# Optimization experiments

Hardware: AMD Instinct MI355X
Metric: run time of the kernel (lower is better)

The kernel has to match this reference:

```python
import jax, jax.numpy as jnp
import numpy as np

N_NODES = 50000
N_EDGES = 800000
N_GRAPHS = 16
F_IN = 128
E_DIM = 16
HID = 32
HEADS = 2
EPS_BN = 1e-5


def gatv2_conv(x, edge_index, edge_attr, Wl, bl, Wr, br, We, att, bias, heads, out_ch):
    """PyG GATv2Conv (share_weights=False, concat=True, add_self_loops=True, fill_value='mean')."""
    n = x.shape[0]
    src, dst = edge_index[0], edge_index[1]
    loop = jnp.arange(n)
    src = jnp.concatenate([src, loop])
    dst = jnp.concatenate([dst, loop])
    ea = jnp.concatenate([edge_attr, jnp.broadcast_to(edge_attr.mean(0), (n, edge_attr.shape[1]))])
    x_l = (x @ Wl + bl).reshape(n, heads, out_ch)   # source transform
    x_r = (x @ Wr + br).reshape(n, heads, out_ch)   # target transform
    e = (ea @ We).reshape(-1, heads, out_ch)
    m = jax.nn.leaky_relu(x_l[src] + x_r[dst] + e, 0.2)      # [E, H, C]
    alpha = (m * att[None]).sum(-1)                          # [E, H]
    amax = jax.ops.segment_max(alpha, dst, num_segments=n)
    ex = jnp.exp(alpha - amax[dst])
    denom = jax.ops.segment_sum(ex, dst, num_segments=n)
    alpha = ex / (denom[dst] + 1e-16)
    out = jax.ops.segment_sum(x_l[src] * alpha[..., None], dst, num_segments=n)
    return out.reshape(n, heads * out_ch) + bias


def batch_norm(x, g, b):
    mu = x.mean(0)
    var = jnp.var(x, axis=0)  # biased, as torch BatchNorm1d training mode
    return (x - mu) * jax.lax.rsqrt(var + EPS_BN) * g + b


def setup_inputs() -> dict:
    key = jax.random.key(0)
    ks = jax.random.split(key, 24)
    s = 0.1
    d1 = HID * HEADS  # 64
    inp = {
        'x': jax.random.normal(ks[0], (N_NODES, F_IN), jnp.float32),
        'edge_index': jax.random.randint(ks[1], (2, N_EDGES), 0, N_NODES),
        'edge_attr': jax.random.normal(ks[2], (N_EDGES, E_DIM), jnp.float32),
        'batch': jnp.sort(jax.random.randint(ks[3], (N_NODES,), 0, N_GRAPHS)),
        'skip1_W': jax.random.normal(ks[4], (F_IN, d1)) * s,
        'skip1_b': jnp.zeros((d1,)),
        'conv1_Wl': jax.random.normal(ks[5], (F_IN, d1)) * s,
        'conv1_bl': jnp.zeros((d1,)),
        'conv1_Wr': jax.random.normal(ks[6], (F_IN, d1)) * s,
        'conv1_br': jnp.zeros((d1,)),
        'conv1_We': jax.random.normal(ks[7], (E_DIM, d1)) * s,
        'conv1_att': jax.random.normal(ks[8], (HEADS, HID)) * s,
        'conv1_bias': jnp.zeros((d1,)),
        'bn1_g': jnp.ones((d1,)),
        'bn1_b': jnp.zeros((d1,)),
        'skip2_W': jax.random.normal(ks[9], (d1, HID)) * s,
        'skip2_b': jnp.zeros((HID,)),
        'conv2_Wl': jax.random.normal(ks[10], (d1, HID)) * s,
        'conv2_bl': jnp.zeros((HID,)),
        'conv2_Wr': jax.random.normal(ks[11], (d1, HID)) * s,
        'conv2_br': jnp.zeros((HID,)),
        'conv2_We': jax.random.normal(ks[12], (E_DIM, HID)) * s,
        'conv2_att': jax.random.normal(ks[13], (1, HID)) * s,
        'conv2_bias': jnp.zeros((HID,)),
        'bn2_g': jnp.ones((HID,)),
        'bn2_b': jnp.zeros((HID,)),
    }
    return inp


def reference(x, edge_index, edge_attr, batch,
              skip1_W, skip1_b, conv1_Wl, conv1_bl, conv1_Wr, conv1_br, conv1_We, conv1_att, conv1_bias, bn1_g, bn1_b,
              skip2_W, skip2_b, conv2_Wl, conv2_bl, conv2_Wr, conv2_br, conv2_We, conv2_att, conv2_bias, bn2_g, bn2_b):
    h_proj = x @ skip1_W + skip1_b
    h = gatv2_conv(x, edge_index, edge_attr, conv1_Wl, conv1_bl, conv1_Wr, conv1_br, conv1_We, conv1_att, conv1_bias, HEADS, HID)
    h = jax.nn.elu(batch_norm(h, bn1_g, bn1_b) + h_proj)
    h_proj = h @ skip2_W + skip2_b
    h2 = gatv2_conv(h, edge_index, edge_attr, conv2_Wl, conv2_bl, conv2_Wr, conv2_br, conv2_We, conv2_att, conv2_bias, 1, HID)
    h2 = jax.nn.elu(batch_norm(h2, bn2_g, bn2_b) + h_proj)
    ones = jnp.ones((h2.shape[0],), h2.dtype)
    counts = jax.ops.segment_sum(ones, batch, num_segments=N_GRAPHS)
    x_mean = jax.ops.segment_sum(h2, batch, num_segments=N_GRAPHS) / jnp.maximum(counts, 1.0)[:, None]
    x_max = jax.ops.segment_max(h2, batch, num_segments=N_GRAPHS)
    x_max = jnp.where(counts[:, None] > 0, x_max, 0.0)
    return jnp.concatenate([x_mean, x_max], axis=1)
```

## Files before the change

kernel.cpp:

```cpp
#include <hip/hip_runtime.h>
#include <hip/hip_bf16.h>

#define NE 800000
#define NN 50000
#define NG 16
#define ETOT (NE + NN)

typedef unsigned short u16;
typedef __attribute__((ext_vector_type(8))) short short8;
typedef __attribute__((ext_vector_type(4))) float float4v;

__device__ __forceinline__ float b2f(u16 u) {
  return __uint_as_float(((unsigned)u) << 16);
}
__device__ __forceinline__ u16 f2b(float f) {
  __hip_bfloat16 b = __float2bfloat16(f);
  return *(u16*)&b;
}
__device__ __forceinline__ void cv8(uint4 v, float* o) {
  o[0] = __uint_as_float(v.x << 16);
  o[1] = __uint_as_float(v.x & 0xFFFF0000u);
  o[2] = __uint_as_float(v.y << 16);
  o[3] = __uint_as_float(v.y & 0xFFFF0000u);
  o[4] = __uint_as_float(v.z << 16);
  o[5] = __uint_as_float(v.z & 0xFFFF0000u);
  o[6] = __uint_as_float(v.w << 16);
  o[7] = __uint_as_float(v.w & 0xFFFF0000u);
}
__device__ __forceinline__ unsigned pk2(float a, float b) {
  return (unsigned)f2b(a) | ((unsigned)f2b(b) << 16);
}
__device__ __forceinline__ unsigned f2key(float f) {
  unsigned u = __float_as_uint(f);
  return (u & 0x80000000u) ? ~u : (u | 0x80000000u);
}
__device__ __forceinline__ float key2f(unsigned k) {
  unsigned u = (k & 0x80000000u) ? (k ^ 0x80000000u) : ~k;
  return __uint_as_float(u);
}
__device__ __forceinline__ int plaus(unsigned h) {
  unsigned eh = (h >> 7) & 0xFF;
  return (h == 0) || (eh >= 100 && eh <= 140);
}
__device__ __forceinline__ float lrelu(float v) {
  return (v > 0.f) ? v : 0.2f * v;
}

__global__ __launch_bounds__(256) void k_init(uint4* __restrict__ zbase, int zcnt16,
                                              const unsigned* __restrict__ a,
                                              const unsigned* __restrict__ b,
                                              const unsigned* __restrict__ c,
                                              int* __restrict__ flags) {
  uint4 z = {0, 0, 0, 0};
  for (int i = blockIdx.x * 256 + threadIdx.x; i < zcnt16; i += gridDim.x * 256)
    zbase[i] = z;
  if (blockIdx.x != 0) return;
  __shared__ int cnt[3];
  if (threadIdx.x < 3) cnt[threadIdx.x] = 0;
  __syncthreads();
  const unsigned* arr[3] = {a, b, c};
  for (int k = 0; k < 3; k++) {
    int ok = 0;
    for (int i = threadIdx.x; i < 4096; i += 256) {
      unsigned w = arr[k][i];
      ok += (plaus(w & 0xFFFFu) && plaus(w >> 16)) ? 1 : 0;
    }
    atomicAdd(&cnt[k], ok);
  }
  __syncthreads();
  if (threadIdx.x == 0) {
    int f0 = cnt[0] > 2048, f1 = cnt[1] > 2048, f2 = cnt[2] > 2048;
    flags[0] = f0;
    flags[1] = f1;
    flags[2] = f2;
    flags[3] = f0 && f1 && f2;
  }
}

__global__ __launch_bounds__(256) void k_histcol(const int* __restrict__ ei,
                                                 const void* __restrict__ ea,
                                                 const int* __restrict__ flg,
                                                 int* __restrict__ deg4,
                                                 float* __restrict__ mean_part) {
  int gt = blockIdx.x * 256 + threadIdx.x;
  if (gt < ETOT) {
    int dst = (gt < NE) ? ei[NE + gt] : gt - NE;
    atomicAdd(&deg4[(blockIdx.x & 3) * NN + dst], 1);
  }
  bool eb = flg[2] != 0;
  int col = gt & 15;
  int row = gt >> 4;
  int rstride = (gridDim.x * 256) >> 4;
  float s = 0.f;
  if (eb) {
    const u16* p = (const u16*)ea;
    for (int e = row; e < NE; e += rstride) s += b2f(p[(size_t)e * 16 + col]);
  } else {
    const float* p = (const float*)ea;
    for (int e = row; e < NE; e += rstride) s += p[(size_t)e * 16 + col];
  }
  __shared__ float ls[256];
  ls[threadIdx.x] = s;
  __syncthreads();
  if (threadIdx.x < 16) {
    float t = 0.f;
    for (int i = threadIdx.x; i < 256; i += 16) t += ls[i];
    atomicAdd(&mean_part[(blockIdx.x & 63) * 16 + threadIdx.x], t);
  }
}

template <int K, int N>
__device__ __forceinline__ void load_W_f32(float* Wf, const void* W, bool wb) {
  if (wb) {
    const u16* Wp = (const u16*)W;
    for (int i = threadIdx.x; i < K * N / 8; i += 256) {
      float t[8];
      cv8(*(const uint4*)(Wp + i * 8), t);
#pragma unroll
      for (int q = 0; q < 8; q++) Wf[i * 8 + q] = t[q];
    }
  } else {
    const float* Wp = (const float*)W;
    for (int i = threadIdx.x; i < K * N / 4; i += 256) {
      float4 v = *(const float4*)(Wp + i * 4);
      Wf[i * 4 + 0] = v.x; Wf[i * 4 + 1] = v.y;
      Wf[i * 4 + 2] = v.z; Wf[i * 4 + 3] = v.w;
    }
  }
}

template <int K, int N, int RPB>
__device__ __forceinline__ void gemm_mfma_tile(
    const float* __restrict__ Wf,
    const void* __restrict__ xin, bool xb, bool wb,
    const void* __restrict__ bb, u16* __restrict__ out, int tile) {
  constexpr int CT = N / 16;
  constexpr int WPC = 4 / CT;
  constexpr int KK = K / 32;
  int lane = threadIdx.x & 63;
  int wave = threadIdx.x >> 6;
  int col = lane & 15;
  int quad = lane >> 4;
  int ct = wave % CT;
  int rt_off = wave / CT;
  short8 bh[KK], bl[KK];
#pragma unroll
  for (int kk = 0; kk < KK; kk++) {
    short8 th, tl;
#pragma unroll
    for (int j = 0; j < 8; j++) {
      float w = Wf[(kk * 32 + quad * 8 + j) * N + ct * 16 + col];
      u16 hb = f2b(w);
      th[j] = (short)hb;
      tl[j] = (short)f2b(w - b2f(hb));
    }
    bh[kk] = th;
    bl[kk] = tl;
  }
  float bias = wb ? b2f(((const u16*)bb)[ct * 16 + col])
                  : ((const float*)bb)[ct * 16 + col];
  int rt0 = tile * RPB;
  for (int i = rt_off; i < RPB; i += WPC) {
    int rt = rt0 + i;
    int row = rt * 16 + col;
    float4v acc = {0.f, 0.f, 0.f, 0.f};
    if (xb) {
      const u16* xp = (const u16*)xin;
#pragma unroll
      for (int kk = 0; kk < KK; kk++) {
        short8 af = *(const short8*)(xp + (size_t)row * K + kk * 32 + quad * 8);
        acc = __builtin_amdgcn_mfma_f32_16x16x32_bf16(af, bh[kk], acc, 0, 0, 0);
        if (!wb)
          acc = __builtin_amdgcn_mfma_f32_16x16x32_bf16(af, bl[kk], acc, 0, 0, 0);
      }
    } else {
      const float* xp = (const float*)xin;
#pragma unroll
      for (int kk = 0; kk < KK; kk++) {
        float4 v0 = *(const float4*)(xp + (size_t)row * K + kk * 32 + quad * 8);
        float4 v1 = *(const float4*)(xp + (size_t)row * K + kk * 32 + quad * 8 + 4);
        float a[8] = {v0.x, v0.y, v0.z, v0.w, v1.x, v1.y, v1.z, v1.w};
        short8 ah, al;
#pragma unroll
        for (int j = 0; j < 8; j++) {
          u16 hb = f2b(a[j]);
          ah[j] = (short)hb;
          al[j] = (short)f2b(a[j] - b2f(hb));
        }
        acc = __builtin_amdgcn_mfma_f32_16x16x32_bf16(ah, bh[kk], acc, 0, 0, 0);
        acc = __builtin_amdgcn_mfma_f32_16x16x32_bf16(al, bh[kk], acc, 0, 0, 0);
        if (!wb)
          acc = __builtin_amdgcn_mfma_f32_16x16x32_bf16(ah, bl[kk], acc, 0, 0, 0);
      }
    }
#pragma unroll
    for (int r = 0; r < 4; r++) {
      int orow = rt * 16 + quad * 4 + r;
      out[(size_t)orow * N + ct * 16 + col] = f2b(acc[r] + bias);
    }
  }
}

template <int K, int N, int TILES, int RPB>
__global__ __launch_bounds__(256) void k_scanlin1(
    const int* __restrict__ deg4, int* __restrict__ start, int* __restrict__ cursor,
    const float* __restrict__ mean_part, float* __restrict__ mean_sums,
    const void* __restrict__ xin, const int* __restrict__ flg,
    const void* W0, const void* W1, const void* W2,
    const void* b0, const void* b1, const void* b2,
    u16* __restrict__ o0, u16* __restrict__ o1, u16* __restrict__ o2, int M) {
  (void)M;
  __shared__ __align__(16) float smem[K * N];

  if ((int)blockIdx.x == 0) {
    int t = threadIdx.x;
    if (t < 16) {
      float s = 0.f;
#pragma unroll
      for (int j = 0; j < 64; j++) s += mean_part[j * 16 + t];
      mean_sums[t] = s;
    }
    constexpr int NT = (NN + 1023) / 1024;
    int* ws = (int*)smem;
    int* tbase = ws + 256;
    int lane = t & 63;
    int wv = t >> 6;
    for (int tile = 0; tile < NT; tile++) {
      int idx = tile * 1024 + t * 4;
      int4 d = {0, 0, 0, 0};
      if (idx + 3 < NN) {
#pragma unroll
        for (int c = 0; c < 4; c++) {
          int4 dc = *(const int4*)(deg4 + c * NN + idx);
          d.x += dc.x; d.y += dc.y; d.z += dc.z; d.w += dc.w;
        }
      } else {
#pragma unroll
        for (int c = 0; c < 4; c++) {
          if (idx + 0 < NN) d.x += deg4[c * NN + idx + 0];
          if (idx + 1 < NN) d.y += deg4[c * NN + idx + 1];
          if (idx + 2 < NN) d.z += deg4[c * NN + idx + 2];
          if (idx + 3 < NN) d.w += deg4[c * NN + idx + 3];
        }
      }
      int s4 = d.x + d.y + d.z + d.w;
      int r = s4;
#pragma unroll
      for (int ofs = 1; ofs < 64; ofs <<= 1) r += __shfl_xor(r, ofs, 64);
      if (lane == 0) ws[tile * 4 + wv] = r;
    }
    __syncthreads();
    if (wv == 0) {
      int g0 = 0, g1 = 0, g2 = 0, g3 = 0;
      if (lane < NT) {
        g0 = ws[lane * 4 + 0];
        g1 = ws[lane * 4 + 1];
        g2 = ws[lane * 4 + 2];
        g3 = ws[lane * 4 + 3];
      }
      int gs = g0 + g1 + g2 + g3;
      int sc = gs;
#pragma unroll
      for (int ofs = 1; ofs < 64; ofs <<= 1) {
        int v = __shfl_up(sc, ofs, 64);
        if (lane >= ofs) sc += v;
      }
      int base = sc - gs;
      if (lane < NT) {
        tbase[lane * 4 + 0] = base;
        tbase[lane * 4 + 1] = base + g0;
        tbase[lane * 4 + 2] = base + g0 + g1;
        tbase[lane * 4 + 3] = base + g0 + g1 + g2;
      }
      if (lane == NT - 1) start[NN] = base + gs;
    }
    __syncthreads();
    for (int tile = 0; tile < NT; tile++) {
      int idx = tile * 1024 + t * 4;
      int4 d = {0, 0, 0, 0};
      if (idx + 3 < NN) {
#pragma unroll
        for (int c = 0; c < 4; c++) {
          int4 dc = *(const int4*)(deg4 + c * NN + idx);
          d.x += dc.x; d.y += dc.y; d.z += dc.z; d.w += dc.w;
        }
      } else {
#pragma unroll
        for (int c = 0; c < 4; c++) {
          if (idx + 0 < NN) d.x += deg4[c * NN + idx + 0];
          if (idx + 1 < NN) d.y += deg4[c * NN + idx + 1];
          if (idx + 2 < NN) d.z += deg4[c * NN + idx + 2];
          if (idx + 3 < NN) d.w += deg4[c * NN + idx + 3];
        }
      }
      int s4 = d.x + d.y + d.z + d.w;
      int sc = s4;
#pragma unroll
      for (int ofs = 1; ofs < 64; ofs <<= 1) {
        int v = __shfl_up(sc, ofs, 64);
        if (lane >= ofs) sc += v;
      }
      int excl = tbase[tile * 4 + wv] + (sc - s4);
      int4 st;
      st.x = excl;
      st.y = excl + d.x;
      st.z = st.y + d.y;
      st.w = st.z + d.z;
      if (idx + 3 < NN) {
        *(int4*)(start + idx) = st;
        *(int4*)(cursor + idx) = st;
      } else {
        if (idx + 0 < NN) { start[idx + 0] = st.x; cursor[idx + 0] = st.x; }
        if (idx + 1 < NN) { start[idx + 1] = st.y; cursor[idx + 1] = st.y; }
        if (idx + 2 < NN) { start[idx + 2] = st.z; cursor[idx + 2] = st.z; }
        if (idx + 3 < NN) { start[idx + 3] = st.w; cursor[idx + 3] = st.w; }
      }
    }
    return;
  }
  int lidx = blockIdx.x - 1;
  int wset = lidx / TILES;
  int tile = lidx % TILES;
  bool wb = flg[1] != 0;
  bool xb = flg[0] != 0;
  const void* W = wset == 0 ? W0 : (wset == 1 ? W1 : W2);
  const void* bb = wset == 0 ? b0 : (wset == 1 ? b1 : b2);
  u16* out = wset == 0 ? o0 : (wset == 1 ? o1 : o2);
  load_W_f32<K, N>(smem, W, wb);
  __syncthreads();
  gemm_mfma_tile<K, N, RPB>(smem, xin, xb, wb, bb, out, tile);
}

__global__ __launch_bounds__(256) void k_buildcsr_pay(
    const int* __restrict__ ei, const void* __restrict__ eattr,
    const int* __restrict__ flg, const float* __restrict__ mean_sums,
    int* __restrict__ cursor, int* __restrict__ csr_src,
    u16* __restrict__ ea16) {
  int e = blockIdx.x * 256 + threadIdx.x;
  if (e >= ETOT) return;
  bool eb = flg[2] != 0;
  int src, dst;
  if (e < NE) { src = ei[e]; dst = ei[NE + e]; } else { src = dst = e - NE; }
  float rec[16];
  if (e < NE) {
    if (eb) {
      const uint4* q = (const uint4*)((const u16*)eattr + (size_t)e * 16);
      cv8(q[0], rec);
      cv8(q[1], rec + 8);
    } else {
      const float* q = (const float*)eattr + (size_t)e * 16;
#pragma unroll
      for (int k = 0; k < 16; k++) rec[k] = q[k];
    }
  } else {
#pragma unroll
    for (int k = 0; k < 16; k++) rec[k] = mean_sums[k] * (1.0f / NE);
  }
  int pos = atomicAdd(&cursor[dst], 1);
  csr_src[pos] = src;
  u16 rb[16];
#pragma unroll
  for (int k = 0; k < 16; k++) rb[k] = f2b(rec[k]);
  uint4* dp = (uint4*)(ea16 + (size_t)pos * 16);
  dp[0] = *(uint4*)rb;
  dp[1] = *(uint4*)(rb + 8);
}

__global__ __launch_bounds__(256) void k_buildcsr(const int* __restrict__ ei,
                                                  int* __restrict__ cursor,
                                                  uint2* __restrict__ csr) {
  int e = blockIdx.x * 256 + threadIdx.x;
  if (e >= ETOT) return;
  int src, dst;
  if (e < NE) { src = ei[e]; dst = ei[NE + e]; } else { src = dst = e - NE; }
  int pos = atomicAdd(&cursor[dst], 1);
  uint2 r; r.x = (unsigned)src; r.y = (unsigned)e;
  csr[pos] = r;
}

__global__ __launch_bounds__(256) void k_ewgemm(
    const u16* __restrict__ ea, const int* __restrict__ flg,
    const void* We1, const void* We2,
    u16* __restrict__ ew1, u16* __restrict__ ew2) {
  bool wb = flg[1] != 0;
  int lane = threadIdx.x & 63;
  int col = lane & 15;
  int quad = lane >> 4;
  short8 b1h[4], b1l[4], b2h[2], b2l[2];
#pragma unroll
  for (int ct = 0; ct < 4; ct++) {
    short8 th, tl;
#pragma unroll
    for (int j = 0; j < 8; j++) {
      int k = quad * 8 + j;
      float w = 0.f;
      if (k < 16)
        w = wb ? b2f(((const u16*)We1)[k * 64 + ct * 16 + col])
               : ((const float*)We1)[k * 64 + ct * 16 + col];
      u16 hb = f2b(w);
      th[j] = (short)hb;
      tl[j] = (short)f2b(w - b2f(hb));
    }
    b1h[ct] = th; b1l[ct] = tl;
  }
#pragma unroll
  for (int ct = 0; ct < 2; ct++) {
    short8 th, tl;
#pragma unroll
    for (int j = 0; j < 8; j++) {
      int k = quad * 8 + j;
      float w = 0.f;
      if (k < 16)
        w = wb ? b2f(((const u16*)We2)[k * 32 + ct * 16 + col])
               : ((const float*)We2)[k * 32 + ct * 16 + col];
      u16 hb = f2b(w);
      th[j] = (short)hb;
      tl[j] = (short)f2b(w - b2f(hb));
    }
    b2h[ct] = th; b2l[ct] = tl;
  }
  int nw = (gridDim.x * 256) >> 6;
  int wid = (blockIdx.x * 256 + threadIdx.x) >> 6;
  const int NT = ETOT / 16;
  for (int rt = wid; rt < NT; rt += nw) {
    int row = rt * 16 + col;
    short8 af = {0, 0, 0, 0, 0, 0, 0, 0};
    if (quad < 2) af = *(const short8*)(ea + (size_t)row * 16 + quad * 8);
#pragma unroll
    for (int ct = 0; ct < 4; ct++) {
      float4v acc = {0.f, 0.f, 0.f, 0.f};
      acc = __builtin_amdgcn_mfma_f32_16x16x32_bf16(af, b1h[ct], acc, 0, 0, 0);
      acc = __builtin_amdgcn_mfma_f32_16x16x32_bf16(af, b1l[ct], acc, 0, 0, 0);
#pragma unroll
      for (int r = 0; r < 4; r++)
        ew1[(size_t)(rt * 16 + quad * 4 + r) * 64 + ct * 16 + col] = f2b(acc[r]);
    }
#pragma unroll
    for (int ct = 0; ct < 2; ct++) {
      float4v acc = {0.f, 0.f, 0.f, 0.f};
      acc = __builtin_amdgcn_mfma_f32_16x16x32_bf16(af, b2h[ct], acc, 0, 0, 0);
      acc = __builtin_amdgcn_mfma_f32_16x16x32_bf16(af, b2l[ct], acc, 0, 0, 0);
#pragma unroll
      for (int r = 0; r < 4; r++)
        ew2[(size_t)(rt * 16 + quad * 4 + r) * 32 + ct * 16 + col] = f2b(acc[r]);
    }
  }
}

template <int K, int N, int RPB>
__global__ __launch_bounds__(256) void k_lin3b(
    const void* __restrict__ xin, const int* __restrict__ flg,
    const void* W0, const void* W1, const void* W2,
    const void* b0, const void* b1, const void* b2,
    u16* __restrict__ o0, u16* __restrict__ o1, u16* __restrict__ o2, int M) {
  (void)M;
  __shared__ __align__(16) float smem[K * N];
  bool wb = flg[1] != 0;
  const void* W = blockIdx.y == 0 ? W0 : (blockIdx.y == 1 ? W1 : W2);
  const void* bb = blockIdx.y == 0 ? b0 : (blockIdx.y == 1 ? b1 : b2);
  u16* out = blockIdx.y == 0 ? o0 : (blockIdx.y == 1 ? o1 : o2);
  load_W_f32<K, N>(smem, W, wb);
  __syncthreads();
  gemm_mfma_tile<K, N, RPB>(smem, xin, true, wb, bb, out, blockIdx.x);
}

__device__ __forceinline__ float dot16b(const u16* __restrict__ p,
                                        const float* __restrict__ W) {
  float ea[16];
  const uint4* q = (const uint4*)p;
  cv8(q[0], ea);
  cv8(q[1], ea + 8);
  float s = 0.f;
#pragma unroll
  for (int k = 0; k < 16; k++) s += ea[k] * W[k];
  return s;
}
__device__ __forceinline__ float dot16u(const u16* __restrict__ p,
                                        const float* __restrict__ W) {
  const uint4* q = (const uint4*)p;
  uint4 A = q[0], B = q[1];
  unsigned w0 = (unsigned)__builtin_amdgcn_readfirstlane((int)A.x);
  unsigned w1 = (unsigned)__builtin_amdgcn_readfirstlane((int)A.y);
  unsigned w2 = (unsigned)__builtin_amdgcn_readfirstlane((int)A.z);
  unsigned w3 = (unsigned)__builtin_amdgcn_readfirstlane((int)A.w);
  unsigned w4 = (unsigned)__builtin_amdgcn_readfirstlane((int)B.x);
  unsigned w5 = (unsigned)__builtin_amdgcn_readfirstlane((int)B.y);
  unsigned w6 = (unsigned)__builtin_amdgcn_readfirstlane((int)B.z);
  unsigned w7 = (unsigned)__builtin_amdgcn_readfirstlane((int)B.w);
  float s = 0.f;
  s += __uint_as_float(w0 << 16) * W[0];
  s += __uint_as_float(w0 & 0xFFFF0000u) * W[1];
  s += __uint_as_float(w1 << 16) * W[2];
  s += __uint_as_float(w1 & 0xFFFF0000u) * W[3];
  s += __uint_as_float(w2 << 16) * W[4];
  s += __uint_as_float(w2 & 0xFFFF0000u) * W[5];
  s += __uint_as_float(w3 << 16) * W[6];
  s += __uint_as_float(w3 & 0xFFFF0000u) * W[7];
  s += __uint_as_float(w4 << 16) * W[8];
  s += __uint_as_float(w4 & 0xFFFF0000u) * W[9];
  s += __uint_as_float(w5 << 16) * W[10];
  s += __uint_as_float(w5 & 0xFFFF0000u) * W[11];
  s += __uint_as_float(w6 << 16) * W[12];
  s += __uint_as_float(w6 & 0xFFFF0000u) * W[13];
  s += __uint_as_float(w7 << 16) * W[14];
  s += __uint_as_float(w7 & 0xFFFF0000u) * W[15];
  return s;
}
__device__ __forceinline__ float dot16f(const float* __restrict__ q,
                                        const float* __restrict__ W) {
  float s = 0.f;
#pragma unroll
  for (int k = 0; k < 16; k++) s += q[k] * W[k];
  return s;
}

template <int H, int C, bool PRE>
__global__ __launch_bounds__(256) void k_fusedp(
    const int* __restrict__ start, const int* __restrict__ csr_src,
    const u16* __restrict__ pay, const u16* __restrict__ ewp,
    const int* __restrict__ flg,
    const u16* __restrict__ xl, const u16* __restrict__ xr,
    const void* We, const void* att, u16* __restrict__ agg) {
  constexpr int D = H * C;
  constexpr int NPW = 64 / D;
  bool wb = flg[1] != 0;
  int lane = threadIdx.x & 63;
  int ch = lane % D;
  float Wreg[16];
  if constexpr (!PRE) {
    if (wb) {
      const u16* Wp = (const u16*)We;
#pragma unroll
      for (int k = 0; k < 16; k++) Wreg[k] = b2f(Wp[k * D + ch]);
    } else {
      const float* Wp = (const float*)We;
#pragma unroll
      for (int k = 0; k < 16; k++) Wreg[k] = Wp[k * D + ch];
    }
  }
  float attv = wb ? b2f(((const u16*)att)[ch]) : ((const float*)att)[ch];
  int wid = (blockIdx.x * 256 + threadIdx.x) >> 6;

  if constexpr (NPW == 1) {
    int node = __builtin_amdgcn_readfirstlane(wid);
    int s0 = __builtin_amdgcn_readfirstlane(start[node]);
    int s1 = __builtin_amdgcn_readfirstlane(start[node + 1]);
    float xrv = b2f(xr[(unsigned)node * D + ch]);
    float ssum = 0.f, acc = 0.f;
    int p = s0;
    for (; p + 3 < s1; p += 4) {
      int c0 = __builtin_amdgcn_readfirstlane(csr_src[p + 0]);
      int c1 = __builtin_amdgcn_readfirstlane(csr_src[p + 1]);
      int c2 = __builtin_amdgcn_readfirstlane(csr_src[p + 2]);
      int c3 = __builtin_amdgcn_readfirstlane(csr_src[p + 3]);
      float xlv0 = b2f(xl[(unsigned)c0 * D + ch]);
      float xlv1 = b2f(xl[(unsigned)c1 * D + ch]);
      float xlv2 = b2f(xl[(unsigned)c2 * D + ch]);
      float xlv3 = b2f(xl[(unsigned)c3 * D + ch]);
      float ev0, ev1, ev2, ev3;
      if constexpr (PRE) {
        ev0 = b2f(ewp[(size_t)(p + 0) * D + ch]);
        ev1 = b2f(ewp[(size_t)(p + 1) * D + ch]);
        ev2 = b2f(ewp[(size_t)(p + 2) * D + ch]);
        ev3 = b2f(ewp[(size_t)(p + 3) * D + ch]);
      } else {
        ev0 = dot16u(pay + (size_t)(p + 0) * 16, Wreg);
        ev1 = dot16u(pay + (size_t)(p + 1) * 16, Wreg);
        ev2 = dot16u(pay + (size_t)(p + 2) * 16, Wreg);
        ev3 = dot16u(pay + (size_t)(p + 3) * 16, Wreg);
      }
      float t0 = lrelu(xlv0 + xrv + ev0) * attv;
      float t1 = lrelu(xlv1 + xrv + ev1) * attv;
      float t2 = lrelu(xlv2 + xrv + ev2) * attv;
      float t3 = lrelu(xlv3 + xrv + ev3) * attv;
#pragma unroll
      for (int mk = 1; mk <= 16; mk <<= 1) {
        t0 += __shfl_xor(t0, mk, 64);
        t1 += __shfl_xor(t1, mk, 64);
        t2 += __shfl_xor(t2, mk, 64);
        t3 += __shfl_xor(t3, mk, 64);
      }
      float ex0 = __expf(t0);
      float ex1 = __expf(t1);
      float ex2 = __expf(t2);
      float ex3 = __expf(t3);
      ssum += (ex0 + ex1) + (ex2 + ex3);
      acc += ex0 * xlv0 + ex1 * xlv1;
      acc += ex2 * xlv2 + ex3 * xlv3;
    }
    for (; p < s1; ++p) {
      int c0 = __builtin_amdgcn_readfirstlane(csr_src[p]);
      float xlv = b2f(xl[(unsigned)c0 * D + ch]);
      float ev;
      if constexpr (PRE) ev = b2f(ewp[(size_t)p * D + ch]);
      else ev = dot16u(pay + (size_t)p * 16, Wreg);
      float t = lrelu(xlv + xrv + ev) * attv;
#pragma unroll
      for (int mk = 1; mk <= 16; mk <<= 1) t += __shfl_xor(t, mk, 64);
      float ex = __expf(t);
      ssum += ex;
      acc += ex * xlv;
    }
    agg[(size_t)node * D + ch] = f2b(acc / (ssum + 1e-16f));
  } else {
    int node = wid * NPW + lane / D;
    int s0 = start[node], s1 = start[node + 1];
    int deg = s1 - s0;
    int last = s1 - 1;
    int degmax = max(deg, __shfl_xor(deg, 32, 64));
    float xrv = b2f(xr[(unsigned)node * D + ch]);
    float ssum = 0.f, acc = 0.f;
    for (int i = 0; i < degmax; i += 4) {
      int p0 = min(s0 + i + 0, last);
      int p1 = min(s0 + i + 1, last);
      int p2 = min(s0 + i + 2, last);
      int p3 = min(s0 + i + 3, last);
      bool a0 = i + 0 < deg, a1 = i + 1 < deg, a2 = i + 2 < deg, a3 = i + 3 < deg;
      int c0 = csr_src[p0];
      int c1 = csr_src[p1];
      int c2 = csr_src[p2];
      int c3 = csr_src[p3];
      float xlv0 = b2f(xl[(unsigned)c0 * D + ch]);
      float xlv1 = b2f(xl[(unsigned)c1 * D + ch]);
      float xlv2 = b2f(xl[(unsigned)c2 * D + ch]);
      float xlv3 = b2f(xl[(unsigned)c3 * D + ch]);
      float ev0, ev1, ev2, ev3;
      if constexpr (PRE) {
        ev0 = b2f(ewp[(size_t)p0 * D + ch]);
        ev1 = b2f(ewp[(size_t)p1 * D + ch]);
        ev2 = b2f(ewp[(size_t)p2 * D + ch]);
        ev3 = b2f(ewp[(size_t)p3 * D + ch]);
      } else {
        ev0 = dot16b(pay + (size_t)p0 * 16, Wreg);
        ev1 = dot16b(pay + (size_t)p1 * 16, Wreg);
        ev2 = dot16b(pay + (size_t)p2 * 16, Wreg);
        ev3 = dot16b(pay + (size_t)p3 * 16, Wreg);
      }
      float t0 = lrelu(xlv0 + xrv + ev0) * attv;
      float t1 = lrelu(xlv1 + xrv + ev1) * attv;
      float t2 = lrelu(xlv2 + xrv + ev2) * attv;
      float t3 = lrelu(xlv3 + xrv + ev3) * attv;
#pragma unroll
      for (int mk = 1; mk <= 16; mk <<= 1) {
        t0 += __shfl_xor(t0, mk, 64);
        t1 += __shfl_xor(t1, mk, 64);
        t2 += __shfl_xor(t2, mk, 64);
        t3 += __shfl_xor(t3, mk, 64);
      }
      float ex0 = a0 ? __expf(t0) : 0.f;
      float ex1 = a1 ? __expf(t1) : 0.f;
      float ex2 = a2 ? __expf(t2) : 0.f;
      float ex3 = a3 ? __expf(t3) : 0.f;
      ssum += (ex0 + ex1) + (ex2 + ex3);
      acc += ex0 * xlv0 + ex1 * xlv1;
      acc += ex2 * xlv2 + ex3 * xlv3;
    }
    agg[(size_t)node * D + ch] = f2b(acc / (ssum + 1e-16f));
  }
}

template <int H, int C>
__global__ __launch_bounds__(256) void k_fusedg(
    const int* __restrict__ start, const uint2* __restrict__ csr,
    const void* __restrict__ eattr, const int* __restrict__ flg,
    const float* __restrict__ mean_sums,
    const u16* __restrict__ xl, const u16* __restrict__ xr,
    const void* We, const void* att, u16* __restrict__ agg) {
  constexpr int D = H * C;
  constexpr int NPW = 64 / D;
  bool wb = flg[1] != 0;
  bool eb = flg[2] != 0;
  int lane = threadIdx.x & 63;
  int ch = lane % D;
  float Wreg[16];
  if (wb) {
    const u16* Wp = (const u16*)We;
#pragma unroll
    for (int k = 0; k < 16; k++) Wreg[k] = b2f(Wp[k * D + ch]);
  } else {
    const float* Wp = (const float*)We;
#pragma unroll
    for (int k = 0; k < 16; k++) Wreg[k] = Wp[k * D + ch];
  }
  float attv = wb ? b2f(((const u16*)att)[ch]) : ((const float*)att)[ch];
  float ev_self = 0.f;
#pragma unroll
  for (int k = 0; k < 16; k++) ev_self += mean_sums[k] * (1.0f / NE) * Wreg[k];
  int wid = (blockIdx.x * 256 + threadIdx.x) >> 6;
  int node = wid * NPW + lane / D;
  int s0 = start[node], s1 = start[node + 1];
  int deg = s1 - s0;
  int last = s1 - 1;
  int degmax = deg;
  if constexpr (NPW == 2) degmax = max(deg, __shfl_xor(deg, 32, 64));
  float xrv = b2f(xr[(size_t)node * D + ch]);
  float ssum = 0.f, acc = 0.f;
  for (int i = 0; i < degmax; i += 2) {
    uint2 cr0 = csr[min(s0 + i, last)];
    uint2 cr1 = csr[min(s0 + i + 1, last)];
    bool a0 = i < deg, a1 = i + 1 < deg;
    float xlv0 = b2f(xl[(size_t)cr0.x * D + ch]);
    float xlv1 = b2f(xl[(size_t)cr1.x * D + ch]);
    float ev0 = cr0.y < NE ? (eb ? dot16b((const u16*)eattr + (size_t)cr0.y * 16, Wreg)
                                 : dot16f((const float*)eattr + (size_t)cr0.y * 16, Wreg))
                           : ev_self;
    float ev1 = cr1.y < NE ? (eb ? dot16b((const u16*)eattr + (size_t)cr1.y * 16, Wreg)
                                 : dot16f((const float*)eattr + (size_t)cr1.y * 16, Wreg))
                           : ev_self;
    float mv0 = xlv0 + xrv + ev0;
    float mv1 = xlv1 + xrv + ev1;
    mv0 = (mv0 > 0.f) ? mv0 : 0.2f * mv0;
    mv1 = (mv1 > 0.f) ? mv1 : 0.2f * mv1;
    float t0 = mv0 * attv, t1 = mv1 * attv;
#pragma unroll
    for (int mk = 1; mk <= 16; mk <<= 1) {
      t0 += __shfl_xor(t0, mk, 64);
      t1 += __shfl_xor(t1, mk, 64);
    }
    float ex0 = a0 ? __expf(t0) : 0.f;
    float ex1 = a1 ? __expf(t1) : 0.f;
    ssum += ex0 + ex1;
    acc += ex0 * xlv0 + ex1 * xlv1;
  }
  agg[(size_t)node * D + ch] = f2b(acc / (ssum + 1e-16f));
}

template <int D>
__global__ __launch_bounds__(256) void k_bnred(const u16* __restrict__ v,
                                               float* __restrict__ sum,
                                               float* __restrict__ sq, int M) {
  constexpr int RB = 256 / D;
  int tid = threadIdx.x;
  int c = tid % D;
  int rg = tid / D;
  float s = 0.f, q = 0.f;
  for (int r = blockIdx.x * RB + rg; r < M; r += gridDim.x * RB) {
    float x = b2f(v[(size_t)r * D + c]);
    s += x;
    q += x * x;
  }
  __shared__ float ls[256], lq[256];
  ls[tid] = s; lq[tid] = q;
  __syncthreads();
  if (tid < D) {
    float ts = 0.f, tq = 0.f;
    for (int i = tid; i < 256; i += D) { ts += ls[i]; tq += lq[i]; }
    atomicAdd(&sum[tid], ts);
    atomicAdd(&sq[tid], tq);
  }
}

template <int D>
__global__ __launch_bounds__(256) void k_bnapply(const u16* __restrict__ agg,
                                                 const u16* __restrict__ hp,
                                                 const float* __restrict__ sum,
                                                 const float* __restrict__ sq,
                                                 const void* g, const void* b,
                                                 const int* __restrict__ flg,
                                                 u16* __restrict__ out, int M) {
  bool wb = flg[1] != 0;
  int idx = blockIdx.x * 256 + threadIdx.x;
  if (idx >= M * D) return;
  int c = idx & (D - 1);
  float gc = wb ? b2f(((const u16*)g)[c]) : ((const float*)g)[c];
  float bc = wb ? b2f(((const u16*)b)[c]) : ((const float*)b)[c];
  float mu = sum[c] * (1.f / M);
  float var = fmaxf(sq[c] * (1.f / M) - mu * mu, 0.f);
  float sc = rsqrtf(var + 1e-5f) * gc;
  float v = (b2f(agg[idx]) - mu) * sc + bc + b2f(hp[idx]);
  v = v > 0.f ? v : expm1f(v);
  out[idx] = f2b(v);
}

__global__ __launch_bounds__(256) void k_poolall(
    const u16* __restrict__ agg2, const u16* __restrict__ hp2,
    const float* __restrict__ sum, const float* __restrict__ sq,
    const void* g, const void* b, const int* __restrict__ flg,
    const int* __restrict__ batch,
    float* __restrict__ pool_sum, unsigned* __restrict__ pool_maxk,
    float* __restrict__ pool_cnt, int* __restrict__ done_cnt,
    void* __restrict__ out) {
  bool wb = flg[1] != 0;
  int c = threadIdx.x & 31;
  int rg = threadIdx.x >> 5;
  float gc = wb ? b2f(((const u16*)g)[c]) : ((const float*)g)[c];
  float bc = wb ? b2f(((const u16*)b)[c]) : ((const float*)b)[c];
  float mu = sum[c] * (1.f / NN);
  float var = fmaxf(sq[c] * (1.f / NN) - mu * mu, 0.f);
  float scl = rsqrtf(var + 1e-5f) * gc;
  float sh = bc - mu * scl;

  const int NPB = 256;
  int n0 = blockIdx.x * NPB;
  int nend = min(n0 + NPB, NN);
  int cur = -1;
  float s = 0.f, mx = 0.f;
  int cnt = 0;
  for (int n = n0 + rg; n < nend; n += 8) {
    int gi = batch[n];
    float v = b2f(agg2[(size_t)n * 32 + c]) * scl + sh + b2f(hp2[(size_t)n * 32 + c]);
    v = v > 0.f ? v : expm1f(v);
    if (gi != cur) {
      if (cur >= 0) {
        atomicAdd(&pool_sum[cur * 32 + c], s);
        atomicMax(&pool_maxk[cur * 32 + c], f2key(mx));
        if (c == 0) atomicAdd(&pool_cnt[cur], (float)cnt);
      }
      cur = gi; s = 0.f; mx = -INFINITY; cnt = 0;
    }
    s += v;
    mx = fmaxf(mx, v);
    cnt++;
  }
  if (cur >= 0) {
    atomicAdd(&pool_sum[cur * 32 + c], s);
    atomicMax(&pool_maxk[cur * 32 + c], f2key(mx));
    if (c == 0) atomicAdd(&pool_cnt[cur], (float)cnt);
  }
  __threadfence();
  __syncthreads();
  __shared__ int lastblk;
  if (threadIdx.x == 0) lastblk = (atomicAdd(done_cnt, 1) == (int)gridDim.x - 1);
  __syncthreads();
  if (!lastblk) return;
  bool ob = flg[3] != 0;
  for (int idx = threadIdx.x; idx < NG * 64; idx += 256) {
    int gi = idx / 64, cc = idx % 64;
    float cntv = atomicAdd(&pool_cnt[gi], 0.f);
    float val;
    if (cc < 32) val = atomicAdd(&pool_sum[gi * 32 + cc], 0.f) / fmaxf(cntv, 1.f);
    else {
      unsigned k = atomicMax(&pool_maxk[gi * 32 + (cc - 32)], 0u);
      val = cntv > 0.f ? key2f(k) : 0.f;
    }
    if (ob) ((u16*)out)[idx] = f2b(val);
    else ((float*)out)[idx] = val;
  }
}

extern "C" void kernel_launch(void* const* d_in, const int* in_sizes, int n_in,
                              void* d_out, int out_size, void* d_ws, size_t ws_size,
                              hipStream_t stream) {
  (void)in_sizes; (void)n_in; (void)out_size;
  const void* x     = d_in[0];
  const int*  ei    = (const int*)d_in[1];
  const void* eattr = d_in[2];
  const int*  batch = (const int*)d_in[3];
  const void* skip1_W = d_in[4];
  const void* skip1_b = d_in[5];
  const void* c1_Wl = d_in[6];
  const void* c1_bl = d_in[7];
  const void* c1_Wr = d_in[8];
  const void* c1_br = d_in[9];
  const void* c1_We = d_in[10];
  const void* c1_att = d_in[11];
  const void* bn1_g = d_in[13];
  const void* bn1_b = d_in[14];
  const void* skip2_W = d_in[15];
  const void* skip2_b = d_in[16];
  const void* c2_Wl = d_in[17];
  const void* c2_bl = d_in[18];
  const void* c2_Wr = d_in[19];
  const void* c2_br = d_in[20];
  const void* c2_We = d_in[21];
  const void* c2_att = d_in[22];
  const void* bn2_g = d_in[24];
  const void* bn2_b = d_in[25];

  float* ws = (float*)d_ws;
  size_t off = 0;
  auto alloc = [&](size_t nfl) {
    float* p = ws + off;
    off += (nfl + 15) & ~(size_t)15;
    return p;
  };
  int*   flags      = (int*)alloc(16);
  float* mean_sums  = alloc(16);
  float* mean_part  = alloc(64 * 16);
  int*   deg4       = (int*)alloc((size_t)4 * NN);
  float* bnsum1     = alloc(64);
  float* bnsq1      = alloc(64);
  float* bnsum2     = alloc(32);
  float* bnsq2      = alloc(32);
  float* pool_cnt   = alloc(NG);
  float* pool_sum   = alloc(NG * 32);
  unsigned* pool_maxk = (unsigned*)alloc(NG * 32);
  int*   done_pool  = (int*)alloc(16);
  size_t zcnt16 = (off * sizeof(float)) / 16;
  size_t zoff = off;

  int* start   = (int*)alloc(NN + 1);
  int* cursor  = (int*)alloc(NN);
  int* csr_src = (int*)alloc(ETOT);
  u16* ea16    = (u16*)alloc((size_t)ETOT * 8);
  u16* ew1     = (u16*)alloc((size_t)ETOT * 32);
  u16* ew2     = (u16*)alloc((size_t)ETOT * 16);
  uint2* csr = nullptr;
  u16* xl1 = (u16*)alloc((size_t)NN * 32);
  u16* xr1 = (u16*)alloc((size_t)NN * 32);
  u16* hp1 = (u16*)alloc((size_t)NN * 32);
  u16* agg = (u16*)alloc((size_t)NN * 32);
  int tier = 0;
  if (off * sizeof(float) > ws_size) {
    tier = 1;
    off = zoff;
    start   = (int*)alloc(NN + 1);
    cursor  = (int*)alloc(NN);
    csr_src = (int*)alloc(ETOT);
    ea16    = (u16*)alloc((size_t)ETOT * 8);
    ew1 = ew2 = nullptr;
    xl1 = (u16*)alloc((size_t)NN * 32);
    xr1 = (u16*)alloc((size_t)NN * 32);
    hp1 = (u16*)alloc((size_t)NN * 32);
    agg = (u16*)alloc((size_t)NN * 32);
  }
  if (tier == 1 && off * sizeof(float) > ws_size) {
    tier = 2;
    off = zoff;
    start   = (int*)alloc(NN + 1);
    cursor  = (int*)alloc(NN);
    csr     = (uint2*)alloc((size_t)ETOT * 2);
    ea16    = nullptr;
    xl1 = (u16*)alloc((size_t)NN * 32);
    xr1 = (u16*)alloc((size_t)NN * 32);
    hp1 = (u16*)alloc((size_t)NN * 32);
    agg = (u16*)alloc((size_t)NN * 32);
  }
  u16* h1  = xr1;
  u16* xl2 = xl1;
  u16* xr2 = xl1 + (size_t)NN * 32;
  u16* hp2 = hp1;

  int eg = (ETOT + 255) / 256;

  k_init<<<128, 256, 0, stream>>>((uint4*)d_ws, (int)zcnt16,
                                  (const unsigned*)x, (const unsigned*)skip1_W,
                                  (const unsigned*)eattr, flags);
  k_histcol<<<eg, 256, 0, stream>>>(ei, eattr, flags, deg4, mean_part);
  k_scanlin1<128, 64, 625, 5><<<1876, 256, 0, stream>>>(
      deg4, start, cursor, mean_part, mean_sums, x, flags, c1_Wl, c1_Wr, skip1_W,
      c1_bl, c1_br, skip1_b, xl1, xr1, hp1, NN);
  if (tier <= 1) {
    k_buildcsr_pay<<<eg, 256, 0, stream>>>(ei, eattr, flags, mean_sums,
                                           cursor, csr_src, ea16);
  } else {
    k_buildcsr<<<eg, 256, 0, stream>>>(ei, cursor, csr);
  }
  if (tier == 0) {
    k_ewgemm<<<1024, 256, 0, stream>>>(ea16, flags, c1_We, c2_We, ew1, ew2);
  }
  if (tier == 0) {
    k_fusedp<2, 32, true><<<NN / 4, 256, 0, stream>>>(start, csr_src, ea16, ew1,
                                                      flags, xl1, xr1, c1_We,
                                                      c1_att, agg);
  } else if (tier == 1) {
    k_fusedp<2, 32, false><<<NN / 4, 256, 0, stream>>>(start, csr_src, ea16, nullptr,
                                                       flags, xl1, xr1, c1_We,
                                                       c1_att, agg);
  } else {
    k_fusedg<2, 32><<<NN / 4, 256, 0, stream>>>(start, csr, eattr, flags, mean_sums,
                                                xl1, xr1, c1_We, c1_att, agg);
  }
  k_bnred<64><<<256, 256, 0, stream>>>(agg, bnsum1, bnsq1, NN);
  k_bnapply<64><<<(NN * 64 + 255) / 256, 256, 0, stream>>>(agg, hp1, bnsum1, bnsq1,
                                                           bn1_g, bn1_b, flags, h1, NN);
  {
    dim3 g(625, 3);
    k_lin3b<64, 32, 5><<<g, 256, 0, stream>>>(h1, flags, c2_Wl, c2_Wr, skip2_W,
                                              c2_bl, c2_br, skip2_b,
                                              xl2, xr2, hp2, NN);
  }
  if (tier == 0) {
    k_fusedp<1, 32, true><<<NN / 8, 256, 0, stream>>>(start, csr_src, ea16, ew2,
                                                      flags, xl2, xr2, c2_We,
                                                      c2_att, agg);
  } else if (tier == 1) {
    k_fusedp<1, 32, false><<<NN / 8, 256, 0, stream>>>(start, csr_src, ea16, nullptr,
                                                       flags, xl2, xr2, c2_We,
                                                       c2_att, agg);
  } else {
    k_fusedg<1, 32><<<NN / 8, 256, 0, stream>>>(start, csr, eattr, flags, mean_sums,
                                                xl2, xr2, c2_We, c2_att, agg);
  }
  k_bnred<32><<<256, 256, 0, stream>>>(agg, bnsum2, bnsq2, NN);
  k_poolall<<<(NN + 255) / 256, 256, 0, stream>>>(agg, hp2, bnsum2, bnsq2,
                                                  bn2_g, bn2_b, flags, batch,
                                                  pool_sum, pool_maxk, pool_cnt,
                                                  done_pool, d_out);
}
```

Before: 577.3 us.

## Pre-split fp32 input into bf16 hi/lo in histogram kernel; drop LDS weight staging

Splitting fp32 x into bf16 hi and lo parts now happens once in k_histcol, which writes two bf16 arrays. The three GEMMs in k_scanlin1 then read those arrays directly instead of each converting x again. The weight matrix is no longer staged through a 32 KB shared-memory buffer with a barrier; each lane reads its weight fragment straight from global memory. This cuts shared-memory use, which should raise occupancy, and removes repeated conversion work. The cost is an extra 25.6 MB written and read back for the split input, and possibly uncoalesced weight loads.

```diff
diff --git a/kernel.cpp b/kernel.cpp
--- a/kernel.cpp
+++ b/kernel.cpp
@@ -79,9 +79,12 @@
 
 __global__ __launch_bounds__(256) void k_histcol(const int* __restrict__ ei,
                                                  const void* __restrict__ ea,
+                                                 const void* __restrict__ xin,
                                                  const int* __restrict__ flg,
                                                  int* __restrict__ deg4,
-                                                 float* __restrict__ mean_part) {
+                                                 float* __restrict__ mean_part,
+                                                 u16* __restrict__ xh,
+                                                 u16* __restrict__ xlo) {
   int gt = blockIdx.x * 256 + threadIdx.x;
   if (gt < ETOT) {
     int dst = (gt < NE) ? ei[NE + gt] : gt - NE;
@@ -107,33 +110,33 @@
     for (int i = threadIdx.x; i < 256; i += 16) t += ls[i];
     atomicAdd(&mean_part[(blockIdx.x & 63) * 16 + threadIdx.x], t);
   }
-}
-
-template <int K, int N>
-__device__ __forceinline__ void load_W_f32(float* Wf, const void* W, bool wb) {
-  if (wb) {
-    const u16* Wp = (const u16*)W;
-    for (int i = threadIdx.x; i < K * N / 8; i += 256) {
-      float t[8];
-      cv8(*(const uint4*)(Wp + i * 8), t);
-#pragma unroll
-      for (int q = 0; q < 8; q++) Wf[i * 8 + q] = t[q];
-    }
-  } else {
-    const float* Wp = (const float*)W;
-    for (int i = threadIdx.x; i < K * N / 4; i += 256) {
-      float4 v = *(const float4*)(Wp + i * 4);
-      Wf[i * 4 + 0] = v.x; Wf[i * 4 + 1] = v.y;
-      Wf[i * 4 + 2] = v.z; Wf[i * 4 + 3] = v.w;
+  if (flg[0] == 0) {
+    const float4* xp4 = (const float4*)xin;
+    const int nch = NN * 32;
+    int stride = gridDim.x * 256;
+    for (int i = gt; i < nch; i += stride) {
+      float4 v = xp4[i];
+      u16 h0 = f2b(v.x), h1 = f2b(v.y), h2 = f2b(v.z), h3 = f2b(v.w);
+      u16 l0 = f2b(v.x - b2f(h0));
+      u16 l1 = f2b(v.y - b2f(h1));
+      u16 l2 = f2b(v.z - b2f(h2));
+      u16 l3 = f2b(v.w - b2f(h3));
+      uint2 ho, lo2;
+      ho.x = (unsigned)h0 | ((unsigned)h1 << 16);
+      ho.y = (unsigned)h2 | ((unsigned)h3 << 16);
+      lo2.x = (unsigned)l0 | ((unsigned)l1 << 16);
+      lo2.y = (unsigned)l2 | ((unsigned)l3 << 16);
+      *(uint2*)(xh + (size_t)i * 4) = ho;
+      *(uint2*)(xlo + (size_t)i * 4) = lo2;
     }
   }
 }
 
 template <int K, int N, int RPB>
-__device__ __forceinline__ void gemm_mfma_tile(
-    const float* __restrict__ Wf,
-    const void* __restrict__ xin, bool xb, bool wb,
-    const void* __restrict__ bb, u16* __restrict__ out, int tile) {
+__device__ __forceinline__ void gemm_direct(
+    const void* __restrict__ W, const void* __restrict__ bb, bool wb,
+    const u16* __restrict__ xh, const u16* __restrict__ xlo, bool has_lo,
+    u16* __restrict__ out, int tile) {
   constexpr int CT = N / 16;
   constexpr int WPC = 4 / CT;
   constexpr int KK = K / 32;
@@ -149,7 +152,9 @@
     short8 th, tl;
 #pragma unroll
     for (int j = 0; j < 8; j++) {
-      float w = Wf[(kk * 32 + quad * 8 + j) * N + ct * 16 + col];
+      int k = kk * 32 + quad * 8 + j;
+      float w = wb ? b2f(((const u16*)W)[k * N + ct * 16 + col])
+                   : ((const float*)W)[k * N + ct * 16 + col];
       u16 hb = f2b(w);
       th[j] = (short)hb;
       tl[j] = (short)f2b(w - b2f(hb));
@@ -164,34 +169,16 @@
     int rt = rt0 + i;
     int row = rt * 16 + col;
     float4v acc = {0.f, 0.f, 0.f, 0.f};
-    if (xb) {
-      const u16* xp = (const u16*)xin;
-#pragma unroll
-      for (int kk = 0; kk < KK; kk++) {
-        short8 af = *(const short8*)(xp + (size_t)row * K + kk * 32 + quad * 8);
-        acc = __builtin_amdgcn_mfma_f32_16x16x32_bf16(af, bh[kk], acc, 0, 0, 0);
-        if (!wb)
-          acc = __builtin_amdgcn_mfma_f32_16x16x32_bf16(af, bl[kk], acc, 0, 0, 0);
-      }
-    } else {
-      const float* xp = (const float*)xin;
-#pragma unroll
-      for (int kk = 0; kk < KK; kk++) {
-        float4 v0 = *(const float4*)(xp + (size_t)row * K + kk * 32 + quad * 8);
-        float4 v1 = *(const float4*)(xp + (size_t)row * K + kk * 32 + quad * 8 + 4);
-        float a[8] = {v0.x, v0.y, v0.z, v0.w, v1.x, v1.y, v1.z, v1.w};
-        short8 ah, al;
-#pragma unroll
-        for (int j = 0; j < 8; j++) {
-          u16 hb = f2b(a[j]);
-          ah[j] = (short)hb;
-          al[j] = (short)f2b(a[j] - b2f(hb));
-        }
-        acc = __builtin_amdgcn_mfma_f32_16x16x32_bf16(ah, bh[kk], acc, 0, 0, 0);
-        acc = __builtin_amdgcn_mfma_f32_16x16x32_bf16(al, bh[kk], acc, 0, 0, 0);
-        if (!wb)
-          acc = __builtin_amdgcn_mfma_f32_16x16x32_bf16(ah, bl[kk], acc, 0, 0, 0);
-      }
+#pragma unroll
+    for (int kk = 0; kk < KK; kk++) {
+      short8 afh = *(const short8*)(xh + (size_t)row * K + kk * 32 + quad * 8);
+      acc = __builtin_amdgcn_mfma_f32_16x16x32_bf16(afh, bh[kk], acc, 0, 0, 0);
+      if (has_lo) {
+        short8 afl = *(const short8*)(xlo + (size_t)row * K + kk * 32 + quad * 8);
+        acc = __builtin_amdgcn_mfma_f32_16x16x32_bf16(afl, bh[kk], acc, 0, 0, 0);
+      }
+      if (!wb)
+        acc = __builtin_amdgcn_mfma_f32_16x16x32_bf16(afh, bl[kk], acc, 0, 0, 0);
     }
 #pragma unroll
     for (int r = 0; r < 4; r++) {
@@ -205,12 +192,13 @@
 __global__ __launch_bounds__(256) void k_scanlin1(
     const int* __restrict__ deg4, int* __restrict__ start, int* __restrict__ cursor,
     const float* __restrict__ mean_part, float* __restrict__ mean_sums,
-    const void* __restrict__ xin, const int* __restrict__ flg,
+    const void* __restrict__ xin, const u16* __restrict__ xh,
+    const u16* __restrict__ xlo, const int* __restrict__ flg,
     const void* W0, const void* W1, const void* W2,
     const void* b0, const void* b1, const void* b2,
     u16* __restrict__ o0, u16* __restrict__ o1, u16* __restrict__ o2, int M) {
   (void)M;
-  __shared__ __align__(16) float smem[K * N];
+  __shared__ __align__(16) int smem[512];
 
   if ((int)blockIdx.x == 0) {
     int t = threadIdx.x;
@@ -221,7 +209,7 @@
       mean_sums[t] = s;
     }
     constexpr int NT = (NN + 1023) / 1024;
-    int* ws = (int*)smem;
+    int* ws = smem;
     int* tbase = ws + 256;
     int lane = t & 63;
     int wv = t >> 6;
@@ -326,9 +314,8 @@
   const void* W = wset == 0 ? W0 : (wset == 1 ? W1 : W2);
   const void* bb = wset == 0 ? b0 : (wset == 1 ? b1 : b2);
   u16* out = wset == 0 ? o0 : (wset == 1 ? o1 : o2);
-  load_W_f32<K, N>(smem, W, wb);
-  __syncthreads();
-  gemm_mfma_tile<K, N, RPB>(smem, xin, xb, wb, bb, out, tile);
+  const u16* ah = xb ? (const u16*)xin : xh;
+  gemm_direct<K, N, RPB>(W, bb, wb, ah, xlo, !xb, out, tile);
 }
 
 __global__ __launch_bounds__(256) void k_buildcsr_pay(
@@ -454,14 +441,12 @@
     const void* b0, const void* b1, const void* b2,
     u16* __restrict__ o0, u16* __restrict__ o1, u16* __restrict__ o2, int M) {
   (void)M;
-  __shared__ __align__(16) float smem[K * N];
   bool wb = flg[1] != 0;
   const void* W = blockIdx.y == 0 ? W0 : (blockIdx.y == 1 ? W1 : W2);
   const void* bb = blockIdx.y == 0 ? b0 : (blockIdx.y == 1 ? b1 : b2);
   u16* out = blockIdx.y == 0 ? o0 : (blockIdx.y == 1 ? o1 : o2);
-  load_W_f32<K, N>(smem, W, wb);
-  __syncthreads();
-  gemm_mfma_tile<K, N, RPB>(smem, xin, true, wb, bb, out, blockIdx.x);
+  gemm_direct<K, N, RPB>(W, bb, wb, (const u16*)xin, nullptr, false, out,
+                         blockIdx.x);
 }
 
 __device__ __forceinline__ float dot16b(const u16* __restrict__ p,
@@ -887,6 +872,8 @@
   unsigned* pool_maxk = (unsigned*)alloc(NG * 32);
   int*   done_pool  = (int*)alloc(16);
   size_t zcnt16 = (off * sizeof(float)) / 16;
+  u16* xh  = (u16*)alloc((size_t)NN * 64);
+  u16* xlo = (u16*)alloc((size_t)NN * 64);
   size_t zoff = off;
 
   int* start   = (int*)alloc(NN + 1);
@@ -936,10 +923,10 @@
   k_init<<<128, 256, 0, stream>>>((uint4*)d_ws, (int)zcnt16,
                                   (const unsigned*)x, (const unsigned*)skip1_W,
                                   (const unsigned*)eattr, flags);
-  k_histcol<<<eg, 256, 0, stream>>>(ei, eattr, flags, deg4, mean_part);
+  k_histcol<<<eg, 256, 0, stream>>>(ei, eattr, x, flags, deg4, mean_part, xh, xlo);
   k_scanlin1<128, 64, 625, 5><<<1876, 256, 0, stream>>>(
-      deg4, start, cursor, mean_part, mean_sums, x, flags, c1_Wl, c1_Wr, skip1_W,
-      c1_bl, c1_br, skip1_b, xl1, xr1, hp1, NN);
+      deg4, start, cursor, mean_part, mean_sums, x, xh, xlo, flags,
+      c1_Wl, c1_Wr, skip1_W, c1_bl, c1_br, skip1_b, xl1, xr1, hp1, NN);
   if (tier <= 1) {
     k_buildcsr_pay<<<eg, 256, 0, stream>>>(ei, eattr, flags, mean_sums,
                                            cursor, csr_src, ea16);
```

After: 589.7 us. 2.2% more time.
